# Kernel tuning notes

Measured on AMD Instinct MI355X. Metric: run time of the kernel, lower is better.

## Reference

```python
import jax, jax.numpy as jnp
import numpy as np
from jax import lax

M = 4      # signature truncation depth (init kwarg m)
D = 6      # path channel dimension
L = 100000 # path length


def _kron(a, b):
    # flat tensor product of two flattened tensor levels
    return (a[:, None] * b[None, :]).ravel()


def signature(x, m):
    """Truncated path signature of x (L, d) up to depth m, flat concat of levels.
    Matches iisignature.sig(x, m): output size d + d^2 + ... + d^m.
    Sequential Chen recursion over path increments via lax.scan."""
    d = x.shape[1]
    dx = x[1:] - x[:-1]  # (L-1, d) increments

    def step(S, v):
        # exp of the linear segment: e[k] = v^{(x)k} / k!
        e = [v]
        for k in range(2, m + 1):
            e.append(_kron(e[-1], v) / k)
        # Chen: S'^k = S^k + e^k + sum_{j=1}^{k-1} S^j (x) e^{k-j}
        newS = []
        for k in range(1, m + 1):
            t = S[k - 1] + e[k - 1]
            for j in range(1, k):
                t = t + _kron(S[j - 1], e[k - 1 - j])
            newS.append(t)
        return tuple(newS), None

    S0 = tuple(jnp.zeros((d ** k,), x.dtype) for k in range(1, m + 1))
    S, _ = lax.scan(step, S0, dx)
    return jnp.concatenate(S)  # (d + d^2 + ... + d^m,)


def setup_inputs() -> dict:
    key = jax.random.key(0)
    # build a realistic path: cumulative sum of small Gaussian increments
    steps = jax.random.normal(key, (L, D), dtype=jnp.float32) * 0.01
    x = jnp.cumsum(steps, axis=0)
    return {"x": x}


def reference(x) -> jnp.ndarray:
    return signature(x, M)
```

## Files before the change

kernel.cpp:

```cpp
#include <hip/hip_runtime.h>

#define SIGSZ 1554
#define PSTRIDE 1600
#define OFF4 0
#define OFF3 1296
#define OFF2 1512
#define OFF1 1548
#define VROWS 64
#define PMAX 4096

typedef float v2f __attribute__((ext_vector_type(2)));

__device__ __forceinline__ v2f vfma2(v2f a, v2f b, v2f c) {
  return __builtin_elementwise_fma(a, b, c);
}
__device__ __forceinline__ v2f splat2(float s) {
  v2f r; r.x = s; r.y = s; return r;
}

__device__ __forceinline__ float sel6(int idx, float a0, float a1, float a2,
                                      float a3, float a4, float a5) {
  float r = a0;
  r = (idx == 1) ? a1 : r;
  r = (idx == 2) ? a2 : r;
  r = (idx == 3) ? a3 : r;
  r = (idx == 4) ? a4 : r;
  r = (idx == 5) ? a5 : r;
  return r;
}

#define DECL4ROW(k) v2f s4_##k##_0 = {0.f, 0.f}, s4_##k##_1 = {0.f, 0.f}, \
                        s4_##k##_2 = {0.f, 0.f};

#define LOADROW(S, row) { \
  const v2f* q_ = (const v2f*)(vs + (row) * 6); \
  S##p0 = q_[0]; S##p1 = q_[1]; S##p2 = q_[2]; \
  S##vi = vs[(row) * 6 + i]; S##vj = vs[(row) * 6 + j]; \
}

#define UPD4K(S, k, gk) { \
  const v2f gk2 = splat2(gk); \
  s4_##k##_0 = vfma2(gk2, S##p0, s4_##k##_0); \
  s4_##k##_1 = vfma2(gk2, S##p1, s4_##k##_1); \
  s4_##k##_2 = vfma2(gk2, S##p2, s4_##k##_2); \
}

#define STEP(S) { \
  const float aa = S##vi * S##vj; \
  const float sv = s1i * S##vj; \
  const float G2 = fmaf(aa, 1.f / 6.f, fmaf(sv, 0.5f, s2)); \
  const float in4 = fmaf(aa, 1.f / 24.f, fmaf(sv, 1.f / 6.f, s2 * 0.5f)); \
  const v2f in42 = splat2(in4), G22 = splat2(G2); \
  const v2f Gp0 = vfma2(in42, S##p0, s3p0); \
  const v2f Gp1 = vfma2(in42, S##p1, s3p1); \
  const v2f Gp2 = vfma2(in42, S##p2, s3p2); \
  s3p0 = vfma2(G22, S##p0, s3p0); \
  s3p1 = vfma2(G22, S##p1, s3p1); \
  s3p2 = vfma2(G22, S##p2, s3p2); \
  UPD4K(S, 0, Gp0.x) UPD4K(S, 1, Gp0.y) UPD4K(S, 2, Gp1.x) \
  UPD4K(S, 3, Gp1.y) UPD4K(S, 4, Gp2.x) UPD4K(S, 5, Gp2.y) \
  s2 = fmaf(fmaf(S##vi, 0.5f, s1i), S##vj, s2); \
  s1i += S##vi; \
}

__global__ __launch_bounds__(64, 4) void sig_chunk(const float* __restrict__ x,
                                                   float* __restrict__ out,
                                                   int n_inc, int chunk_len) {
  __shared__ alignas(16) float vs[VROWS * 6];
  const int c = blockIdx.x;
  const int p = threadIdx.x;
  const int t0 = c * chunk_len;
  int t1 = t0 + chunk_len; if (t1 > n_inc) t1 = n_inc;
  const int steps = (t1 > t0) ? (t1 - t0) : 0;
  const int pc = (p < 36) ? p : 35;
  const int i = pc / 6, j = pc % 6;
  const bool act = (p < 36);

  const int nv = steps * 6;
  const float* xb = x + (size_t)t0 * 6;
  for (int idx = p; idx < nv; idx += 64) vs[idx] = xb[idx + 6] - xb[idx];
  for (int idx = nv + p; idx < nv + 18; idx += 64) vs[idx] = 0.f;
  __syncthreads();

  DECL4ROW(0) DECL4ROW(1) DECL4ROW(2) DECL4ROW(3) DECL4ROW(4) DECL4ROW(5)
  v2f s3p0 = {0.f, 0.f}, s3p1 = {0.f, 0.f}, s3p2 = {0.f, 0.f};
  float s1i = 0.f, s2 = 0.f;

  v2f Ap0, Ap1, Ap2; float Avi, Avj;
  v2f Bp0, Bp1, Bp2; float Bvi, Bvj;
  LOADROW(A, 0)
  LOADROW(B, 1)
  const int steps_up = (steps + 1) & ~1;
  for (int r = 0; r < steps_up; r += 2) {
    STEP(A)
    LOADROW(A, r + 2)
    STEP(B)
    LOADROW(B, r + 3)
  }

  float* st = out + (size_t)c * PSTRIDE;
  if (act) {
    float4* o4 = (float4*)(st + OFF4 + pc * 36);
    float4 w;
    w.x = s4_0_0.x; w.y = s4_0_0.y; w.z = s4_0_1.x; w.w = s4_0_1.y; o4[0] = w;
    w.x = s4_0_2.x; w.y = s4_0_2.y; w.z = s4_1_0.x; w.w = s4_1_0.y; o4[1] = w;
    w.x = s4_1_1.x; w.y = s4_1_1.y; w.z = s4_1_2.x; w.w = s4_1_2.y; o4[2] = w;
    w.x = s4_2_0.x; w.y = s4_2_0.y; w.z = s4_2_1.x; w.w = s4_2_1.y; o4[3] = w;
    w.x = s4_2_2.x; w.y = s4_2_2.y; w.z = s4_3_0.x; w.w = s4_3_0.y; o4[4] = w;
    w.x = s4_3_1.x; w.y = s4_3_1.y; w.z = s4_3_2.x; w.w = s4_3_2.y; o4[5] = w;
    w.x = s4_4_0.x; w.y = s4_4_0.y; w.z = s4_4_1.x; w.w = s4_4_1.y; o4[6] = w;
    w.x = s4_4_2.x; w.y = s4_4_2.y; w.z = s4_5_0.x; w.w = s4_5_0.y; o4[7] = w;
    w.x = s4_5_1.x; w.y = s4_5_1.y; w.z = s4_5_2.x; w.w = s4_5_2.y; o4[8] = w;
    st[OFF3 + pc * 6 + 0] = s3p0.x;
    st[OFF3 + pc * 6 + 1] = s3p0.y;
    st[OFF3 + pc * 6 + 2] = s3p1.x;
    st[OFF3 + pc * 6 + 3] = s3p1.y;
    st[OFF3 + pc * 6 + 4] = s3p2.x;
    st[OFF3 + pc * 6 + 5] = s3p2.y;
    st[OFF2 + pc] = s2;
    if (j == 0) st[OFF1 + i] = s1i;
  }
}


#define DECLSET(S)                                                  \
  float S##b4_0, S##b4_1, S##b4_2, S##b4_3, S##b4_4, S##b4_5;       \
  float S##b3r_0, S##b3r_1, S##b3r_2, S##b3r_3, S##b3r_4, S##b3r_5; \
  float S##b2r_0, S##b2r_1, S##b2r_2, S##b2r_3, S##b2r_4, S##b2r_5; \
  float S##b1_0, S##b1_1, S##b1_2, S##b1_3, S##b1_4, S##b1_5;       \
  float S##b2ij, S##b2jk, S##b3ijk, S##b1k, S##b1j;

#define LOADSET(S, bp) {                                            \
  const float2* q4 = (const float2*)((bp) + oB4);                   \
  float2 u0 = q4[0], u1 = q4[1], u2 = q4[2];                        \
  S##b4_0 = u0.x; S##b4_1 = u0.y; S##b4_2 = u1.x;                   \
  S##b4_3 = u1.y; S##b4_4 = u2.x; S##b4_5 = u2.y;                   \
  const float2* q3 = (const float2*)((bp) + oB3r);                  \
  float2 w0 = q3[0], w1 = q3[1], w2 = q3[2];                        \
  S##b3r_0 = w0.x; S##b3r_1 = w0.y; S##b3r_2 = w1.x;                \
  S##b3r_3 = w1.y; S##b3r_4 = w2.x; S##b3r_5 = w2.y;                \
  const float2* q2 = (const float2*)((bp) + oB2r);                  \
  float2 y0 = q2[0], y1 = q2[1], y2 = q2[2];                        \
  S##b2r_0 = y0.x; S##b2r_1 = y0.y; S##b2r_2 = y1.x;                \
  S##b2r_3 = y1.y; S##b2r_4 = y2.x; S##b2r_5 = y2.y;                \
  const float2* q1 = (const float2*)((bp) + OFF1);                  \
  float2 z0 = q1[0], z1 = q1[1], z2 = q1[2];                        \
  S##b1_0 = z0.x; S##b1_1 = z0.y; S##b1_2 = z1.x;                   \
  S##b1_3 = z1.y; S##b1_4 = z2.x; S##b1_5 = z2.y;                   \
  S##b2ij = (bp)[oB2ij]; S##b2jk = (bp)[oB2jk];                     \
  S##b3ijk = (bp)[oB3ijk];                                          \
  S##b1k = (bp)[oB1k]; S##b1j = (bp)[oB1j];                         \
}

#define PROD(S) {                                                   \
  const float a1i = sel6(i_, a1_0, a1_1, a1_2, a1_3, a1_4, a1_5);   \
  a4_0 = fmaf(a3, S##b1_0, fmaf(a2, S##b2r_0,                       \
         fmaf(a1i, S##b3r_0, a4_0 + S##b4_0)));                     \
  a4_1 = fmaf(a3, S##b1_1, fmaf(a2, S##b2r_1,                       \
         fmaf(a1i, S##b3r_1, a4_1 + S##b4_1)));                     \
  a4_2 = fmaf(a3, S##b1_2, fmaf(a2, S##b2r_2,                       \
         fmaf(a1i, S##b3r_2, a4_2 + S##b4_2)));                     \
  a4_3 = fmaf(a3, S##b1_3, fmaf(a2, S##b2r_3,                       \
         fmaf(a1i, S##b3r_3, a4_3 + S##b4_3)));                     \
  a4_4 = fmaf(a3, S##b1_4, fmaf(a2, S##b2r_4,                       \
         fmaf(a1i, S##b3r_4, a4_4 + S##b4_4)));                     \
  a4_5 = fmaf(a3, S##b1_5, fmaf(a2, S##b2r_5,                       \
         fmaf(a1i, S##b3r_5, a4_5 + S##b4_5)));                     \
  a3 = fmaf(a2, S##b1k, fmaf(a1i, S##b2jk, a3 + S##b3ijk));         \
  a2 = fmaf(a1i, S##b1j, a2 + S##b2ij);                             \
  a1_0 += S##b1_0; a1_1 += S##b1_1; a1_2 += S##b1_2;                \
  a1_3 += S##b1_3; a1_4 += S##b1_4; a1_5 += S##b1_5;                \
}

__global__ __launch_bounds__(256, 1) void sig_combine(const float* __restrict__ in,
                                                      float* __restrict__ out,
                                                      int n_total, int group,
                                                      int final_out) {
  const int b = blockIdx.x;
  const int p = threadIdx.x;
  const int start = b * group;
  int end = start + group; if (end > n_total) end = n_total;
  const int tc = (p < 216) ? p : 215;
  const bool act = (p < 216);
  const int k_ = tc % 6;
  const int ij = tc / 6;
  const int j_ = ij % 6;
  const int i_ = ij / 6;

  const int oB4 = OFF4 + tc * 6;
  const int oB3r = OFF3 + (j_ * 6 + k_) * 6;
  const int oB2r = OFF2 + k_ * 6;
  const int oB2ij = OFF2 + ij;
  const int oB2jk = OFF2 + j_ * 6 + k_;
  const int oB3ijk = OFF3 + tc;
  const int oB1k = OFF1 + k_;
  const int oB1j = OFF1 + j_;

  const float* sp0 = in + (size_t)start * PSTRIDE;
  float a4_0, a4_1, a4_2, a4_3, a4_4, a4_5;
  {
    const float2* q4 = (const float2*)(sp0 + oB4);
    float2 u0 = q4[0], u1 = q4[1], u2 = q4[2];
    a4_0 = u0.x; a4_1 = u0.y; a4_2 = u1.x;
    a4_3 = u1.y; a4_4 = u2.x; a4_5 = u2.y;
  }
  float a3 = sp0[oB3ijk];
  float a2 = sp0[oB2ij];
  float a1_0, a1_1, a1_2, a1_3, a1_4, a1_5;
  {
    const float2* q1 = (const float2*)(sp0 + OFF1);
    float2 z0 = q1[0], z1 = q1[1], z2 = q1[2];
    a1_0 = z0.x; a1_1 = z0.y; a1_2 = z1.x;
    a1_3 = z1.y; a1_4 = z2.x; a1_5 = z2.y;
  }

  DECLSET(A)
  DECLSET(B)

  int s = start + 1;
  {
    const int sa = (s < end) ? s : (end - 1);
    LOADSET(A, in + (size_t)sa * PSTRIDE)
    const int sb = (s + 1 < end) ? (s + 1) : (end - 1);
    LOADSET(B, in + (size_t)sb * PSTRIDE)
  }
  while (s + 1 < end) {
    PROD(A)
    {
      const int sn = (s + 2 < end) ? (s + 2) : (end - 1);
      LOADSET(A, in + (size_t)sn * PSTRIDE)
    }
    PROD(B)
    {
      const int sn = (s + 3 < end) ? (s + 3) : (end - 1);
      LOADSET(B, in + (size_t)sn * PSTRIDE)
    }
    s += 2;
  }
  if (s < end) { PROD(A) }

  const float a1p = sel6(p, a1_0, a1_1, a1_2, a1_3, a1_4, a1_5);
  if (final_out) {
    float* o = out;
    if (act) {
      float2* o2 = (float2*)(o + 258 + tc * 6);
      float2 w;
      w.x = a4_0; w.y = a4_1; o2[0] = w;
      w.x = a4_2; w.y = a4_3; o2[1] = w;
      w.x = a4_4; w.y = a4_5; o2[2] = w;
      o[42 + tc] = a3;
      if (k_ == 0) o[6 + ij] = a2;
    }
    if (p < 6) o[p] = a1p;
  } else {
    float* st = out + (size_t)b * PSTRIDE;
    if (act) {
      float2* o2 = (float2*)(st + oB4);
      float2 w;
      w.x = a4_0; w.y = a4_1; o2[0] = w;
      w.x = a4_2; w.y = a4_3; o2[1] = w;
      w.x = a4_4; w.y = a4_5; o2[2] = w;
      st[oB3ijk] = a3;
      if (k_ == 0) st[oB2ij] = a2;
    }
    if (p < 6) st[OFF1 + p] = a1p;
  }
}

extern "C" void kernel_launch(void* const* d_in, const int* in_sizes, int n_in,
                              void* d_out, int out_size, void* d_ws, size_t ws_size,
                              hipStream_t stream) {
  const float* x = (const float*)d_in[0];
  const int Lrows = in_sizes[0] / 6;
  const int n_inc = Lrows - 1;

  int P = PMAX;
  int chunk_len = (n_inc + P - 1) / P;
  if (chunk_len > VROWS - 3) {
    chunk_len = VROWS - 3;
    P = (n_inc + chunk_len - 1) / chunk_len;
  }

  float* ws0 = (float*)d_ws;
  float* ws1 = ws0 + (size_t)PMAX * PSTRIDE;

  sig_chunk<<<P, 64, 0, stream>>>(x, ws0, n_inc, chunk_len);

  float* cur = ws0;
  float* other = ws1;
  int n = P;
  while (n > 1) {
    const int g = (n <= 16) ? n : 16;
    const int nb = (n + g - 1) / g;
    const int fin = (nb == 1);
    sig_combine<<<nb, 256, 0, stream>>>(cur, fin ? (float*)d_out : other, n, g, fin);
    float* t = cur; cur = other; other = t;
    n = nb;
  }
}
```

Before: 98.42 us.

## Fuse chunk and combine stages into one cooperative kernel with grid syncs

Replaces the separate chunk kernel and the chain of combine launches with a single cooperative kernel. Each 256-thread block runs four wavefront-level chunks over 1024 slots of up to 98 steps each, then performs a fixed three-level tree combine (16, 8, 8) separated by grid.sync. This removes several kernel launches and their gaps, at the cost of grid-wide barriers, longer per-chunk sequential work, and a combine tree hardcoded to 1024 slots.

New measurement: 249.4 us. +153.4%, slower.

```diff
diff --git a/kernel.cpp b/kernel.cpp
--- a/kernel.cpp
+++ b/kernel.cpp
@@ -1,4 +1,5 @@
 #include <hip/hip_runtime.h>
+#include <hip/hip_cooperative_groups.h>
 
 #define SIGSZ 1554
 #define PSTRIDE 1600
@@ -6,8 +7,10 @@
 #define OFF3 1296
 #define OFF2 1512
 #define OFF1 1548
-#define VROWS 64
-#define PMAX 4096
+#define VROWS 104
+#define NSLOTS 1024
+
+namespace cg = cooperative_groups;
 
 typedef float v2f __attribute__((ext_vector_type(2)));
 
@@ -33,9 +36,9 @@
                         s4_##k##_2 = {0.f, 0.f};
 
 #define LOADROW(S, row) { \
-  const v2f* q_ = (const v2f*)(vs + (row) * 6); \
+  const v2f* q_ = (const v2f*)(vsw + (row) * 6); \
   S##p0 = q_[0]; S##p1 = q_[1]; S##p2 = q_[2]; \
-  S##vi = vs[(row) * 6 + i]; S##vj = vs[(row) * 6 + j]; \
+  S##vi = vsw[(row) * 6 + i]; S##vj = vsw[(row) * 6 + j]; \
 }
 
 #define UPD4K(S, k, gk) { \
@@ -62,66 +65,6 @@
   s2 = fmaf(fmaf(S##vi, 0.5f, s1i), S##vj, s2); \
   s1i += S##vi; \
 }
-
-__global__ __launch_bounds__(64, 4) void sig_chunk(const float* __restrict__ x,
-                                                   float* __restrict__ out,
-                                                   int n_inc, int chunk_len) {
-  __shared__ alignas(16) float vs[VROWS * 6];
-  const int c = blockIdx.x;
-  const int p = threadIdx.x;
-  const int t0 = c * chunk_len;
-  int t1 = t0 + chunk_len; if (t1 > n_inc) t1 = n_inc;
-  const int steps = (t1 > t0) ? (t1 - t0) : 0;
-  const int pc = (p < 36) ? p : 35;
-  const int i = pc / 6, j = pc % 6;
-  const bool act = (p < 36);
-
-  const int nv = steps * 6;
-  const float* xb = x + (size_t)t0 * 6;
-  for (int idx = p; idx < nv; idx += 64) vs[idx] = xb[idx + 6] - xb[idx];
-  for (int idx = nv + p; idx < nv + 18; idx += 64) vs[idx] = 0.f;
-  __syncthreads();
-
-  DECL4ROW(0) DECL4ROW(1) DECL4ROW(2) DECL4ROW(3) DECL4ROW(4) DECL4ROW(5)
-  v2f s3p0 = {0.f, 0.f}, s3p1 = {0.f, 0.f}, s3p2 = {0.f, 0.f};
-  float s1i = 0.f, s2 = 0.f;
-
-  v2f Ap0, Ap1, Ap2; float Avi, Avj;
-  v2f Bp0, Bp1, Bp2; float Bvi, Bvj;
-  LOADROW(A, 0)
-  LOADROW(B, 1)
-  const int steps_up = (steps + 1) & ~1;
-  for (int r = 0; r < steps_up; r += 2) {
-    STEP(A)
-    LOADROW(A, r + 2)
-    STEP(B)
-    LOADROW(B, r + 3)
-  }
-
-  float* st = out + (size_t)c * PSTRIDE;
-  if (act) {
-    float4* o4 = (float4*)(st + OFF4 + pc * 36);
-    float4 w;
-    w.x = s4_0_0.x; w.y = s4_0_0.y; w.z = s4_0_1.x; w.w = s4_0_1.y; o4[0] = w;
-    w.x = s4_0_2.x; w.y = s4_0_2.y; w.z = s4_1_0.x; w.w = s4_1_0.y; o4[1] = w;
-    w.x = s4_1_1.x; w.y = s4_1_1.y; w.z = s4_1_2.x; w.w = s4_1_2.y; o4[2] = w;
-    w.x = s4_2_0.x; w.y = s4_2_0.y; w.z = s4_2_1.x; w.w = s4_2_1.y; o4[3] = w;
-    w.x = s4_2_2.x; w.y = s4_2_2.y; w.z = s4_3_0.x; w.w = s4_3_0.y; o4[4] = w;
-    w.x = s4_3_1.x; w.y = s4_3_1.y; w.z = s4_3_2.x; w.w = s4_3_2.y; o4[5] = w;
-    w.x = s4_4_0.x; w.y = s4_4_0.y; w.z = s4_4_1.x; w.w = s4_4_1.y; o4[6] = w;
-    w.x = s4_4_2.x; w.y = s4_4_2.y; w.z = s4_5_0.x; w.w = s4_5_0.y; o4[7] = w;
-    w.x = s4_5_1.x; w.y = s4_5_1.y; w.z = s4_5_2.x; w.w = s4_5_2.y; o4[8] = w;
-    st[OFF3 + pc * 6 + 0] = s3p0.x;
-    st[OFF3 + pc * 6 + 1] = s3p0.y;
-    st[OFF3 + pc * 6 + 2] = s3p1.x;
-    st[OFF3 + pc * 6 + 3] = s3p1.y;
-    st[OFF3 + pc * 6 + 4] = s3p2.x;
-    st[OFF3 + pc * 6 + 5] = s3p2.y;
-    st[OFF2 + pc] = s2;
-    if (j == 0) st[OFF1 + i] = s1i;
-  }
-}
-
 
 #define DECLSET(S)                                                  \
   float S##b4_0, S##b4_1, S##b4_2, S##b4_3, S##b4_4, S##b4_5;       \
@@ -172,14 +115,10 @@
   a1_3 += S##b1_3; a1_4 += S##b1_4; a1_5 += S##b1_5;                \
 }
 
-__global__ __launch_bounds__(256, 1) void sig_combine(const float* __restrict__ in,
-                                                      float* __restrict__ out,
-                                                      int n_total, int group,
-                                                      int final_out) {
-  const int b = blockIdx.x;
-  const int p = threadIdx.x;
-  const int start = b * group;
-  int end = start + group; if (end > n_total) end = n_total;
+__device__ __forceinline__ void combine_fold(const float* __restrict__ in,
+                                             float* __restrict__ outp,
+                                             int start, int end, int p,
+                                             int final_out) {
   const int tc = (p < 216) ? p : 215;
   const bool act = (p < 216);
   const int k_ = tc % 6;
@@ -241,7 +180,7 @@
 
   const float a1p = sel6(p, a1_0, a1_1, a1_2, a1_3, a1_4, a1_5);
   if (final_out) {
-    float* o = out;
+    float* o = outp;
     if (act) {
       float2* o2 = (float2*)(o + 258 + tc * 6);
       float2 w;
@@ -253,7 +192,7 @@
     }
     if (p < 6) o[p] = a1p;
   } else {
-    float* st = out + (size_t)b * PSTRIDE;
+    float* st = outp;
     if (act) {
       float2* o2 = (float2*)(st + oB4);
       float2 w;
@@ -267,6 +206,94 @@
   }
 }
 
+__global__ __launch_bounds__(256, 1) void sig_all(
+    const float* __restrict__ x, float* __restrict__ ws0,
+    float* __restrict__ ws1, float* __restrict__ ws2,
+    float* __restrict__ out, int n_inc, int chunk_len) {
+  cg::grid_group grid = cg::this_grid();
+  __shared__ alignas(16) float vs[4 * VROWS * 6];
+
+  {
+    const int w = threadIdx.x >> 6;
+    const int lane = threadIdx.x & 63;
+    const int c = blockIdx.x * 4 + w;
+    float* vsw = vs + w * (VROWS * 6);
+
+    const int t0 = c * chunk_len;
+    int t1 = t0 + chunk_len; if (t1 > n_inc) t1 = n_inc;
+    const int steps = (t1 > t0) ? (t1 - t0) : 0;
+    const int pc = (lane < 36) ? lane : 35;
+    const int i = pc / 6, j = pc % 6;
+    const bool act = (lane < 36);
+
+    const int nv = steps * 6;
+    const float* xb = x + (size_t)t0 * 6;
+    for (int idx = lane; idx < nv; idx += 64) vsw[idx] = xb[idx + 6] - xb[idx];
+    for (int idx = nv + lane; idx < nv + 18; idx += 64) vsw[idx] = 0.f;
+    __syncthreads();
+
+    DECL4ROW(0) DECL4ROW(1) DECL4ROW(2) DECL4ROW(3) DECL4ROW(4) DECL4ROW(5)
+    v2f s3p0 = {0.f, 0.f}, s3p1 = {0.f, 0.f}, s3p2 = {0.f, 0.f};
+    float s1i = 0.f, s2 = 0.f;
+
+    v2f Ap0, Ap1, Ap2; float Avi, Avj;
+    v2f Bp0, Bp1, Bp2; float Bvi, Bvj;
+    LOADROW(A, 0)
+    LOADROW(B, 1)
+    const int steps_up = (steps + 1) & ~1;
+    for (int r = 0; r < steps_up; r += 2) {
+      STEP(A)
+      LOADROW(A, r + 2)
+      STEP(B)
+      LOADROW(B, r + 3)
+    }
+
+    float* st = ws0 + (size_t)c * PSTRIDE;
+    if (act) {
+      float4* o4 = (float4*)(st + OFF4 + pc * 36);
+      float4 wq;
+      wq.x = s4_0_0.x; wq.y = s4_0_0.y; wq.z = s4_0_1.x; wq.w = s4_0_1.y; o4[0] = wq;
+      wq.x = s4_0_2.x; wq.y = s4_0_2.y; wq.z = s4_1_0.x; wq.w = s4_1_0.y; o4[1] = wq;
+      wq.x = s4_1_1.x; wq.y = s4_1_1.y; wq.z = s4_1_2.x; wq.w = s4_1_2.y; o4[2] = wq;
+      wq.x = s4_2_0.x; wq.y = s4_2_0.y; wq.z = s4_2_1.x; wq.w = s4_2_1.y; o4[3] = wq;
+      wq.x = s4_2_2.x; wq.y = s4_2_2.y; wq.z = s4_3_0.x; wq.w = s4_3_0.y; o4[4] = wq;
+      wq.x = s4_3_1.x; wq.y = s4_3_1.y; wq.z = s4_3_2.x; wq.w = s4_3_2.y; o4[5] = wq;
+      wq.x = s4_4_0.x; wq.y = s4_4_0.y; wq.z = s4_4_1.x; wq.w = s4_4_1.y; o4[6] = wq;
+      wq.x = s4_4_2.x; wq.y = s4_4_2.y; wq.z = s4_5_0.x; wq.w = s4_5_0.y; o4[7] = wq;
+      wq.x = s4_5_1.x; wq.y = s4_5_1.y; wq.z = s4_5_2.x; wq.w = s4_5_2.y; o4[8] = wq;
+      st[OFF3 + pc * 6 + 0] = s3p0.x;
+      st[OFF3 + pc * 6 + 1] = s3p0.y;
+      st[OFF3 + pc * 6 + 2] = s3p1.x;
+      st[OFF3 + pc * 6 + 3] = s3p1.y;
+      st[OFF3 + pc * 6 + 4] = s3p2.x;
+      st[OFF3 + pc * 6 + 5] = s3p2.y;
+      st[OFF2 + pc] = s2;
+      if (j == 0) st[OFF1 + i] = s1i;
+    }
+  }
+
+  __threadfence();
+  grid.sync();
+
+  if (blockIdx.x < 64) {
+    combine_fold(ws0, ws1 + (size_t)blockIdx.x * PSTRIDE,
+                 blockIdx.x * 16, blockIdx.x * 16 + 16, threadIdx.x, 0);
+  }
+  __threadfence();
+  grid.sync();
+
+  if (blockIdx.x < 8) {
+    combine_fold(ws1, ws2 + (size_t)blockIdx.x * PSTRIDE,
+                 blockIdx.x * 8, blockIdx.x * 8 + 8, threadIdx.x, 0);
+  }
+  __threadfence();
+  grid.sync();
+
+  if (blockIdx.x == 0) {
+    combine_fold(ws2, out, 0, 8, threadIdx.x, 1);
+  }
+}
+
 extern "C" void kernel_launch(void* const* d_in, const int* in_sizes, int n_in,
                               void* d_out, int out_size, void* d_ws, size_t ws_size,
                               hipStream_t stream) {
@@ -274,27 +301,16 @@
   const int Lrows = in_sizes[0] / 6;
   const int n_inc = Lrows - 1;
 
-  int P = PMAX;
-  int chunk_len = (n_inc + P - 1) / P;
-  if (chunk_len > VROWS - 3) {
-    chunk_len = VROWS - 3;
-    P = (n_inc + chunk_len - 1) / chunk_len;
-  }
+  int chunk_len = (n_inc + NSLOTS - 1) / NSLOTS;
+  if (chunk_len < 1) chunk_len = 1;
 
   float* ws0 = (float*)d_ws;
-  float* ws1 = ws0 + (size_t)PMAX * PSTRIDE;
-
-  sig_chunk<<<P, 64, 0, stream>>>(x, ws0, n_inc, chunk_len);
-
-  float* cur = ws0;
-  float* other = ws1;
-  int n = P;
-  while (n > 1) {
-    const int g = (n <= 16) ? n : 16;
-    const int nb = (n + g - 1) / g;
-    const int fin = (nb == 1);
-    sig_combine<<<nb, 256, 0, stream>>>(cur, fin ? (float*)d_out : other, n, g, fin);
-    float* t = cur; cur = other; other = t;
-    n = nb;
-  }
-}
+  float* ws1 = ws0 + (size_t)NSLOTS * PSTRIDE;
+  float* ws2 = ws1 + (size_t)64 * PSTRIDE;
+  float* o = (float*)d_out;
+
+  void* args[] = {(void*)&x, (void*)&ws0, (void*)&ws1, (void*)&ws2,
+                  (void*)&o, (void*)&n_inc, (void*)&chunk_len};
+  hipLaunchCooperativeKernel((const void*)sig_all, dim3(256), dim3(256),
+                             args, 0, stream);
+}
```
